# Kernel tuning notes

Hardware: AMD Instinct MI355X
Metric: run time of the kernel (lower is better)

Reference implementation:

```python
import jax, jax.numpy as jnp
import numpy as np

N = 8  # node_count, complete graph
# edge list exactly as in __init__: all (i, j) with i != j, row-major order
_edges = np.array([[i, j] for i in range(N) for j in range(N) if i != j], dtype=np.int32)
SRC = jnp.asarray(_edges[:, 0])  # edge_index[0]
DST = jnp.asarray(_edges[:, 1])  # edge_index[1]


def gcn_norm_adj(edge_w):
    """Dense normalized adjacency D^-1/2 (A + I) D^-1/2 with edge weights, as in PyG GCNConv."""
    A = jnp.zeros((N, N), edge_w.dtype).at[DST, SRC].set(edge_w) + jnp.eye(N, dtype=edge_w.dtype)
    deg = A.sum(axis=1)  # in-degree (weights into each target node, incl. self loop)
    dinv = jnp.where(deg > 0, deg ** -0.5, 0.0)
    return dinv[:, None] * A * dinv[None, :]


def setup_inputs() -> dict:
    key = jax.random.key(0)
    ks = jax.random.split(key, 4)
    B, F_, H, O = 8192, 512, 256, 128
    return {
        "latent_vec": jax.random.normal(ks[0], (B, F_), jnp.float32),
        "node_features": jax.random.normal(ks[1], (N, F_), jnp.float32) * 0.1,
        "edge_attr": jnp.ones((N * (N - 1), 1), jnp.float32),
        "W1": jax.random.normal(ks[2], (F_, H), jnp.float32) / np.sqrt(F_),
        "b1": jnp.zeros((H,), jnp.float32),
        "W2": jax.random.normal(ks[3], (H, O), jnp.float32) / np.sqrt(H),
        "b2": jnp.zeros((O,), jnp.float32),
    }


def reference(latent_vec, node_features, edge_attr, W1, b1, W2, b2):
    # update_graph_with_latent: per-sample softmax perturbation of shared node features
    w = jax.nn.softmax(latent_vec[:, :N], axis=1)[..., None]        # [B, N, 1]
    X = node_features[None, :, :] + 0.1 * w                          # [B, N, F]
    A_hat = gcn_norm_adj(edge_attr[:, 0])                            # [N, N], shared across batch
    # GCNConv1 + ReLU (dropout is identity in eval mode)
    h = jax.nn.relu(jnp.einsum('ij,bjh->bih', A_hat, X @ W1) + b1)   # [B, N, H]
    # GCNConv2
    o = jnp.einsum('ij,bjo->bio', A_hat, h @ W2) + b2                # [B, N, O]
    return o.mean(axis=1)                                            # [B, O]
```

## Files before the change

kernel.cpp:

```cpp
#include <hip/hip_runtime.h>

#define NNODE 8
#define FDIM 512
#define HDIM 256
#define ODIM 128
#define BATCH 8192
#define NEDGE (NNODE * (NNODE - 1))

#define FBLOCKS 8
#define FS (FDIM / FBLOCKS)
#define SPB 16


__global__ __launch_bounds__(256) void gnn_stage(const float* __restrict__ nf,
                                                 const float* __restrict__ W1,
                                                 float* __restrict__ ws) {
    const int k = blockIdx.x;
    const int t = threadIdx.x;
    __shared__ float nf_s[NNODE][FS];

    for (int idx = t; idx < NNODE * FS; idx += 256) {
        int n = idx / FS, f = idx % FS;
        nf_s[n][f] = nf[n * FDIM + k * FS + f];
    }
    __syncthreads();

    float s1 = 0.f;
    float y[NNODE];
#pragma unroll
    for (int n = 0; n < NNODE; n++) y[n] = 0.f;

    for (int ff = 0; ff < FS; ff++) {
        float wf = W1[(k * FS + ff) * HDIM + t];
        s1 += wf;
#pragma unroll
        for (int n = 0; n < NNODE; n++) y[n] = fmaf(nf_s[n][ff], wf, y[n]);
    }

    float* p = ws + (size_t)k * 9 * HDIM;
#pragma unroll
    for (int n = 0; n < NNODE; n++) p[n * HDIM + t] = y[n];
    p[8 * HDIM + t] = s1;
}

__global__ __launch_bounds__(256) void gnn_main(const float* __restrict__ latent,
                                                const float* __restrict__ edge_attr,
                                                const float* __restrict__ b1,
                                                const float* __restrict__ W2,
                                                const float* __restrict__ b2,
                                                const float* __restrict__ ws,
                                                float* __restrict__ out) {
    const int t = threadIdx.x;
    const int bs = blockIdx.x * SPB;

    __shared__ float Ahat_s[NNODE][NNODE];
    __shared__ float m_s[NNODE];
    __shared__ float w_s[SPB][NNODE];
    __shared__ float c_s[SPB][NNODE];
    __shared__ float g_s[SPB][HDIM];

    if (t == 0) {
        float A[NNODE][NNODE];
        for (int i = 0; i < NNODE; i++)
            for (int j = 0; j < NNODE; j++) A[i][j] = (i == j) ? 1.f : 0.f;
        for (int e = 0; e < NEDGE; e++) {
            int i = e / (NNODE - 1);
            int jj = e % (NNODE - 1);
            int j = jj + (jj >= i ? 1 : 0);
            A[j][i] += edge_attr[e];
        }
        float dinv[NNODE];
        for (int i = 0; i < NNODE; i++) {
            float d = 0.f;
            for (int j = 0; j < NNODE; j++) d += A[i][j];
            dinv[i] = d > 0.f ? 1.0f / sqrtf(d) : 0.f;
        }
        for (int i = 0; i < NNODE; i++)
            for (int j = 0; j < NNODE; j++) Ahat_s[i][j] = dinv[i] * A[i][j] * dinv[j];
        for (int j = 0; j < NNODE; j++) {
            float mm = 0.f;
            for (int i = 0; i < NNODE; i++) mm += Ahat_s[i][j];
            m_s[j] = mm * (1.0f / NNODE);
        }
    }

    if (t < SPB * NNODE) {
        int s = t >> 3, j = t & 7;
        w_s[s][j] = latent[(size_t)(bs + s) * FDIM + j];
    }
    __syncthreads();

    float wv = 0.f;
    if (t < SPB * NNODE) {
        int s = t >> 3, j = t & 7;
        float mx = -1e30f;
#pragma unroll
        for (int q = 0; q < NNODE; q++) mx = fmaxf(mx, w_s[s][q]);
        float sum = 0.f;
#pragma unroll
        for (int q = 0; q < NNODE; q++) sum += expf(w_s[s][q] - mx);
        wv = expf(w_s[s][j] - mx) / sum;
    }
    __syncthreads();
    if (t < SPB * NNODE) {
        int s = t >> 3, j = t & 7;
        w_s[s][j] = wv;
    }
    __syncthreads();

    if (t < SPB * NNODE) {
        int s = t >> 3, i = t & 7;
        float c = 0.f;
#pragma unroll
        for (int j = 0; j < NNODE; j++) c = fmaf(Ahat_s[i][j], w_s[s][j], c);
        c_s[s][i] = c;
    }
    __syncthreads();

    float Pj[NNODE];
    float s1t;
    {
        float y[NNODE];
        float s1 = 0.f;
#pragma unroll
        for (int n = 0; n < NNODE; n++) y[n] = 0.f;
        for (int k = 0; k < FBLOCKS; k++) {
            const float* p = ws + (size_t)k * 9 * HDIM;
#pragma unroll
            for (int n = 0; n < NNODE; n++) y[n] += p[n * HDIM + t];
            s1 += p[8 * HDIM + t];
        }
        s1t = s1;
        float bb = b1[t];
#pragma unroll
        for (int j = 0; j < NNODE; j++) {
            float acc = bb;
#pragma unroll
            for (int n = 0; n < NNODE; n++) acc = fmaf(Ahat_s[j][n], y[n], acc);
            Pj[j] = acc;
        }
    }

    {
        float s1t01 = 0.1f * s1t;
        float mreg[NNODE];
#pragma unroll
        for (int j = 0; j < NNODE; j++) mreg[j] = m_s[j];
        for (int s = 0; s < SPB; s++) {
            float g = 0.f;
#pragma unroll
            for (int j = 0; j < NNODE; j++) {
                float pre = fmaf(s1t01, c_s[s][j], Pj[j]);
                g = fmaf(mreg[j], fmaxf(pre, 0.f), g);
            }
            g_s[s][t] = g;
        }
    }
    __syncthreads();

    const int o = t & (ODIM - 1);
    const int grp = t >> 7;
    float acc[8];
#pragma unroll
    for (int k2 = 0; k2 < 8; k2++) acc[k2] = 0.f;

    for (int h = 0; h < HDIM; h += 4) {
        float w0 = W2[(h + 0) * ODIM + o];
        float w1 = W2[(h + 1) * ODIM + o];
        float w2v = W2[(h + 2) * ODIM + o];
        float w3 = W2[(h + 3) * ODIM + o];
#pragma unroll
        for (int k2 = 0; k2 < 8; k2++) {
            const float4 gv = *(const float4*)&g_s[grp * 8 + k2][h];
            acc[k2] = fmaf(gv.x, w0,
                      fmaf(gv.y, w1,
                      fmaf(gv.z, w2v,
                      fmaf(gv.w, w3, acc[k2]))));
        }
    }

    float bo = b2[o];
#pragma unroll
    for (int k2 = 0; k2 < 8; k2++) {
        out[(size_t)(bs + grp * 8 + k2) * ODIM + o] = acc[k2] + bo;
    }
}

extern "C" void kernel_launch(void* const* d_in, const int* in_sizes, int n_in,
                              void* d_out, int out_size, void* d_ws, size_t ws_size,
                              hipStream_t stream) {
    const float* latent = (const float*)d_in[0];
    const float* nf     = (const float*)d_in[1];
    const float* ea     = (const float*)d_in[2];
    const float* W1     = (const float*)d_in[3];
    const float* b1     = (const float*)d_in[4];
    const float* W2     = (const float*)d_in[5];
    const float* b2     = (const float*)d_in[6];
    float* out = (float*)d_out;
    float* ws  = (float*)d_ws;

    hipLaunchKernelGGL(gnn_stage, dim3(FBLOCKS), dim3(256), 0, stream, nf, W1, ws);
    hipLaunchKernelGGL(gnn_main, dim3(BATCH / SPB), dim3(256), 0, stream,
                       latent, ea, b1, W2, b2, ws, out);
}
```

Baseline: 29.05 us.

## Hoist batch-invariant GCN precompute into mid kernel and tile W2 GEMM in LDS

Adds a single-block kernel that computes the normalized adjacency, column means, the reduction of partial products and the bias-adjusted P terms once. Previously each of the 512 main blocks repeated this work, including a serial thread-0 adjacency build. The main kernel now loads these precomputed values, fuses softmax with the adjacency product, and runs the final GEMM with W2 tiles staged in shared memory. Each thread computes a 2-sample by 4-output tile with float4 loads and stores. The stage kernel is also split into more feature blocks. The cost is an extra launch and a serial single-block kernel, plus 32KB of LDS per main block, which may lower occupancy.

```diff
diff --git a/kernel.cpp b/kernel.cpp
--- a/kernel.cpp
+++ b/kernel.cpp
@@ -7,10 +7,15 @@
 #define BATCH 8192
 #define NEDGE (NNODE * (NNODE - 1))
 
-#define FBLOCKS 8
+#define FBLOCKS 16
 #define FS (FDIM / FBLOCKS)
 #define SPB 16
 
+#define WS2_OFF (FBLOCKS * 9 * HDIM)
+#define WS2_P 0
+#define WS2_S1 (8 * HDIM)
+#define WS2_A (WS2_S1 + HDIM)
+#define WS2_M (WS2_A + 64)
 
 __global__ __launch_bounds__(256) void gnn_stage(const float* __restrict__ nf,
                                                  const float* __restrict__ W1,
@@ -19,8 +24,8 @@
     const int t = threadIdx.x;
     __shared__ float nf_s[NNODE][FS];
 
-    for (int idx = t; idx < NNODE * FS; idx += 256) {
-        int n = idx / FS, f = idx % FS;
+    {
+        int n = t >> 5, f = t & 31;
         nf_s[n][f] = nf[n * FDIM + k * FS + f];
     }
     __syncthreads();
@@ -30,6 +35,7 @@
 #pragma unroll
     for (int n = 0; n < NNODE; n++) y[n] = 0.f;
 
+#pragma unroll
     for (int ff = 0; ff < FS; ff++) {
         float wf = W1[(k * FS + ff) * HDIM + t];
         s1 += wf;
@@ -43,22 +49,23 @@
     p[8 * HDIM + t] = s1;
 }
 
-__global__ __launch_bounds__(256) void gnn_main(const float* __restrict__ latent,
-                                                const float* __restrict__ edge_attr,
-                                                const float* __restrict__ b1,
-                                                const float* __restrict__ W2,
-                                                const float* __restrict__ b2,
-                                                const float* __restrict__ ws,
-                                                float* __restrict__ out) {
+__global__ __launch_bounds__(256) void gnn_mid(const float* __restrict__ edge_attr,
+                                               const float* __restrict__ b1,
+                                               float* __restrict__ ws) {
     const int t = threadIdx.x;
-    const int bs = blockIdx.x * SPB;
-
-    __shared__ float Ahat_s[NNODE][NNODE];
+    float y[NNODE];
+    float s1 = 0.f;
+#pragma unroll
+    for (int n = 0; n < NNODE; n++) y[n] = 0.f;
+    for (int k = 0; k < FBLOCKS; k++) {
+        const float* p = ws + (size_t)k * 9 * HDIM;
+#pragma unroll
+        for (int n = 0; n < NNODE; n++) y[n] += p[n * HDIM + t];
+        s1 += p[8 * HDIM + t];
+    }
+
+    __shared__ float A_s[NNODE * NNODE];
     __shared__ float m_s[NNODE];
-    __shared__ float w_s[SPB][NNODE];
-    __shared__ float c_s[SPB][NNODE];
-    __shared__ float g_s[SPB][HDIM];
-
     if (t == 0) {
         float A[NNODE][NNODE];
         for (int i = 0; i < NNODE; i++)
@@ -76,81 +83,85 @@
             dinv[i] = d > 0.f ? 1.0f / sqrtf(d) : 0.f;
         }
         for (int i = 0; i < NNODE; i++)
-            for (int j = 0; j < NNODE; j++) Ahat_s[i][j] = dinv[i] * A[i][j] * dinv[j];
+            for (int j = 0; j < NNODE; j++) A_s[i * NNODE + j] = dinv[i] * A[i][j] * dinv[j];
         for (int j = 0; j < NNODE; j++) {
             float mm = 0.f;
-            for (int i = 0; i < NNODE; i++) mm += Ahat_s[i][j];
+            for (int i = 0; i < NNODE; i++) mm += A_s[i * NNODE + j];
             m_s[j] = mm * (1.0f / NNODE);
         }
     }
-
-    if (t < SPB * NNODE) {
-        int s = t >> 3, j = t & 7;
-        w_s[s][j] = latent[(size_t)(bs + s) * FDIM + j];
-    }
-    __syncthreads();
-
-    float wv = 0.f;
-    if (t < SPB * NNODE) {
-        int s = t >> 3, j = t & 7;
-        float mx = -1e30f;
-#pragma unroll
-        for (int q = 0; q < NNODE; q++) mx = fmaxf(mx, w_s[s][q]);
-        float sum = 0.f;
-#pragma unroll
-        for (int q = 0; q < NNODE; q++) sum += expf(w_s[s][q] - mx);
-        wv = expf(w_s[s][j] - mx) / sum;
-    }
-    __syncthreads();
-    if (t < SPB * NNODE) {
-        int s = t >> 3, j = t & 7;
-        w_s[s][j] = wv;
-    }
+    __syncthreads();
+
+    float* w2 = ws + WS2_OFF;
+    float bb = b1[t];
+#pragma unroll
+    for (int j = 0; j < NNODE; j++) {
+        float acc = bb;
+#pragma unroll
+        for (int n = 0; n < NNODE; n++) acc = fmaf(A_s[j * NNODE + n], y[n], acc);
+        w2[WS2_P + j * HDIM + t] = acc;
+    }
+    w2[WS2_S1 + t] = s1;
+    if (t < NNODE * NNODE) w2[WS2_A + t] = A_s[t];
+    if (t < NNODE) w2[WS2_M + t] = m_s[t];
+}
+
+__global__ __launch_bounds__(256) void gnn_main(const float* __restrict__ latent,
+                                                const float* __restrict__ W2,
+                                                const float* __restrict__ b2,
+                                                const float* __restrict__ ws,
+                                                float* __restrict__ out) {
+    const int t = threadIdx.x;
+    const int bs = blockIdx.x * SPB;
+    const float* wsp = ws + WS2_OFF;
+
+    __shared__ float A_s[NNODE * NNODE];
+    __shared__ float m_s[NNODE];
+    __shared__ float lat_s[SPB][NNODE];
+    __shared__ float c_s[SPB][NNODE];
+    __shared__ float g_s[SPB][HDIM];
+    __shared__ float wt[64 * ODIM];
+
+    if (t < NNODE * NNODE) A_s[t] = wsp[WS2_A + t];
+    if (t >= 64 && t < 64 + NNODE) m_s[t - 64] = wsp[WS2_M + (t - 64)];
+    if (t >= 128 && t < 128 + SPB * NNODE) {
+        int u = t - 128;
+        int s = u >> 3, j = u & 7;
+        lat_s[s][j] = latent[(size_t)(bs + s) * FDIM + j];
+    }
+    float P[NNODE];
+#pragma unroll
+    for (int j = 0; j < NNODE; j++) P[j] = wsp[WS2_P + j * HDIM + t];
+    float s1t = wsp[WS2_S1 + t];
     __syncthreads();
 
     if (t < SPB * NNODE) {
         int s = t >> 3, i = t & 7;
-        float c = 0.f;
-#pragma unroll
-        for (int j = 0; j < NNODE; j++) c = fmaf(Ahat_s[i][j], w_s[s][j], c);
-        c_s[s][i] = c;
-    }
-    __syncthreads();
-
-    float Pj[NNODE];
-    float s1t;
+        float mx = -1e30f;
+#pragma unroll
+        for (int q = 0; q < NNODE; q++) mx = fmaxf(mx, lat_s[s][q]);
+        float sum = 0.f, acc = 0.f;
+#pragma unroll
+        for (int q = 0; q < NNODE; q++) {
+            float e = expf(lat_s[s][q] - mx);
+            sum += e;
+            acc = fmaf(A_s[i * NNODE + q], e, acc);
+        }
+        c_s[s][i] = acc / sum;
+    }
+    __syncthreads();
+
     {
-        float y[NNODE];
-        float s1 = 0.f;
-#pragma unroll
-        for (int n = 0; n < NNODE; n++) y[n] = 0.f;
-        for (int k = 0; k < FBLOCKS; k++) {
-            const float* p = ws + (size_t)k * 9 * HDIM;
-#pragma unroll
-            for (int n = 0; n < NNODE; n++) y[n] += p[n * HDIM + t];
-            s1 += p[8 * HDIM + t];
-        }
-        s1t = s1;
-        float bb = b1[t];
-#pragma unroll
-        for (int j = 0; j < NNODE; j++) {
-            float acc = bb;
-#pragma unroll
-            for (int n = 0; n < NNODE; n++) acc = fmaf(Ahat_s[j][n], y[n], acc);
-            Pj[j] = acc;
-        }
-    }
-
-    {
-        float s1t01 = 0.1f * s1t;
+        float s101 = 0.1f * s1t;
         float mreg[NNODE];
 #pragma unroll
         for (int j = 0; j < NNODE; j++) mreg[j] = m_s[j];
+#pragma unroll 4
         for (int s = 0; s < SPB; s++) {
             float g = 0.f;
 #pragma unroll
             for (int j = 0; j < NNODE; j++) {
-                float pre = fmaf(s1t01, c_s[s][j], Pj[j]);
+                float pre = fmaf(s101, c_s[s][j], P[j]);
                 g = fmaf(mreg[j], fmaxf(pre, 0.f), g);
             }
             g_s[s][t] = g;
@@ -158,32 +169,56 @@
     }
     __syncthreads();
 
-    const int o = t & (ODIM - 1);
-    const int grp = t >> 7;
-    float acc[8];
-#pragma unroll
-    for (int k2 = 0; k2 < 8; k2++) acc[k2] = 0.f;
-
-    for (int h = 0; h < HDIM; h += 4) {
-        float w0 = W2[(h + 0) * ODIM + o];
-        float w1 = W2[(h + 1) * ODIM + o];
-        float w2v = W2[(h + 2) * ODIM + o];
-        float w3 = W2[(h + 3) * ODIM + o];
-#pragma unroll
-        for (int k2 = 0; k2 < 8; k2++) {
-            const float4 gv = *(const float4*)&g_s[grp * 8 + k2][h];
-            acc[k2] = fmaf(gv.x, w0,
-                      fmaf(gv.y, w1,
-                      fmaf(gv.z, w2v,
-                      fmaf(gv.w, w3, acc[k2]))));
-        }
-    }
-
-    float bo = b2[o];
-#pragma unroll
-    for (int k2 = 0; k2 < 8; k2++) {
-        out[(size_t)(bs + grp * 8 + k2) * ODIM + o] = acc[k2] + bo;
-    }
+    const int oq = t & 31;
+    const int sg = t >> 5;
+    const int sa = sg * 2, sb = sg * 2 + 1;
+    float4 acc0 = {0.f, 0.f, 0.f, 0.f};
+    float4 acc1 = {0.f, 0.f, 0.f, 0.f};
+    const float4* W2v = (const float4*)W2;
+    float4* wtv = (float4*)wt;
+
+    for (int tile = 0; tile < HDIM / 64; ++tile) {
+#pragma unroll
+        for (int i = 0; i < 8; ++i)
+            wtv[t + 256 * i] = W2v[tile * 2048 + t + 256 * i];
+        __syncthreads();
+
+#pragma unroll
+        for (int hh = 0; hh < 64; hh += 4) {
+            const int hb = tile * 64 + hh;
+            float4 ga = *(const float4*)&g_s[sa][hb];
+            float4 gb = *(const float4*)&g_s[sb][hb];
+            float4 w0 = *(const float4*)&wt[(hh + 0) * ODIM + oq * 4];
+            float4 w1 = *(const float4*)&wt[(hh + 1) * ODIM + oq * 4];
+            float4 w2r = *(const float4*)&wt[(hh + 2) * ODIM + oq * 4];
+            float4 w3 = *(const float4*)&wt[(hh + 3) * ODIM + oq * 4];
+
+            acc0.x = fmaf(ga.x, w0.x, acc0.x); acc0.y = fmaf(ga.x, w0.y, acc0.y);
+            acc0.z = fmaf(ga.x, w0.z, acc0.z); acc0.w = fmaf(ga.x, w0.w, acc0.w);
+            acc0.x = fmaf(ga.y, w1.x, acc0.x); acc0.y = fmaf(ga.y, w1.y, acc0.y);
+            acc0.z = fmaf(ga.y, w1.z, acc0.z); acc0.w = fmaf(ga.y, w1.w, acc0.w);
+            acc0.x = fmaf(ga.z, w2r.x, acc0.x); acc0.y = fmaf(ga.z, w2r.y, acc0.y);
+            acc0.z = fmaf(ga.z, w2r.z, acc0.z); acc0.w = fmaf(ga.z, w2r.w, acc0.w);
+            acc0.x = fmaf(ga.w, w3.x, acc0.x); acc0.y = fmaf(ga.w, w3.y, acc0.y);
+            acc0.z = fmaf(ga.w, w3.z, acc0.z); acc0.w = fmaf(ga.w, w3.w, acc0.w);
+
+            acc1.x = fmaf(gb.x, w0.x, acc1.x); acc1.y = fmaf(gb.x, w0.y, acc1.y);
+            acc1.z = fmaf(gb.x, w0.z, acc1.z); acc1.w = fmaf(gb.x, w0.w, acc1.w);
+            acc1.x = fmaf(gb.y, w1.x, acc1.x); acc1.y = fmaf(gb.y, w1.y, acc1.y);
+            acc1.z = fmaf(gb.y, w1.z, acc1.z); acc1.w = fmaf(gb.y, w1.w, acc1.w);
+            acc1.x = fmaf(gb.z, w2r.x, acc1.x); acc1.y = fmaf(gb.z, w2r.y, acc1.y);
+            acc1.z = fmaf(gb.z, w2r.z, acc1.z); acc1.w = fmaf(gb.z, w2r.w, acc1.w);
+            acc1.x = fmaf(gb.w, w3.x, acc1.x); acc1.y = fmaf(gb.w, w3.y, acc1.y);
+            acc1.z = fmaf(gb.w, w3.z, acc1.z); acc1.w = fmaf(gb.w, w3.w, acc1.w);
+        }
+        __syncthreads();
+    }
+
+    float4 bo = *(const float4*)&b2[oq * 4];
+    acc0.x += bo.x; acc0.y += bo.y; acc0.z += bo.z; acc0.w += bo.w;
+    acc1.x += bo.x; acc1.y += bo.y; acc1.z += bo.z; acc1.w += bo.w;
+    *(float4*)&out[(size_t)(bs + sa) * ODIM + oq * 4] = acc0;
+    *(float4*)&out[(size_t)(bs + sb) * ODIM + oq * 4] = acc1;
 }
 
 extern "C" void kernel_launch(void* const* d_in, const int* in_sizes, int n_in,
@@ -200,6 +235,7 @@
     float* ws  = (float*)d_ws;
 
     hipLaunchKernelGGL(gnn_stage, dim3(FBLOCKS), dim3(256), 0, stream, nf, W1, ws);
+    hipLaunchKernelGGL(gnn_mid, dim3(1), dim3(256), 0, stream, ea, b1, ws);
     hipLaunchKernelGGL(gnn_main, dim3(BATCH / SPB), dim3(256), 0, stream,
-                       latent, ea, b1, W2, b2, ws, out);
-}
+                       latent, W2, b2, ws, out);
+}
```

Result: no change. 29.01 us (-0.1%).

## Precompute piecewise-linear ReLU breakpoint tables and replace per-sample GEMM with lookups

Applied to the files above, without the earlier changes.

Uses the fact that each hidden pre-activation is affine in a per-sample scalar c_j, so the ReLU pattern depends only on where c_j falls among 256 sorted breakpoints. A new build kernel sorts the breakpoints per node and precomputes prefix-sum tables of W2 contributions for every breakpoint interval. The main kernel then does a softmax, a binary search per node and eight table lookups per output instead of the 256x128 W2 matmul. This trades the main GEMM for a serial build kernel of only 8 blocks, a large workspace table and gather loads. The prefix accumulation over sorted breakpoints can also shift floating-point rounding.

```diff
diff --git a/kernel.cpp b/kernel.cpp
--- a/kernel.cpp
+++ b/kernel.cpp
@@ -5,12 +5,18 @@
 #define HDIM 256
 #define ODIM 128
 #define BATCH 8192
-#define NEDGE (NNODE * (NNODE - 1))
-
-#define FBLOCKS 8
+#define NEDGE 56
+#define FBLOCKS 16
 #define FS (FDIM / FBLOCKS)
 #define SPB 16
-
+#define NBLK (BATCH / SPB)
+
+#define OFF_PART 0
+#define OFF_TAU  (FBLOCKS * 9 * HDIM)
+#define OFF_AHAT (OFF_TAU + NNODE * HDIM)
+#define OFF_TABA (OFF_AHAT + 128)
+#define TABJ     (257 * ODIM)
+#define OFF_TABB (OFF_TABA + NNODE * TABJ)
 
 __global__ __launch_bounds__(256) void gnn_stage(const float* __restrict__ nf,
                                                  const float* __restrict__ W1,
@@ -19,8 +25,8 @@
     const int t = threadIdx.x;
     __shared__ float nf_s[NNODE][FS];
 
-    for (int idx = t; idx < NNODE * FS; idx += 256) {
-        int n = idx / FS, f = idx % FS;
+    {
+        int n = t >> 5, f = t & 31;
         nf_s[n][f] = nf[n * FDIM + k * FS + f];
     }
     __syncthreads();
@@ -30,6 +36,7 @@
 #pragma unroll
     for (int n = 0; n < NNODE; n++) y[n] = 0.f;
 
+#pragma unroll
     for (int ff = 0; ff < FS; ff++) {
         float wf = W1[(k * FS + ff) * HDIM + t];
         s1 += wf;
@@ -43,146 +50,179 @@
     p[8 * HDIM + t] = s1;
 }
 
+__global__ __launch_bounds__(256) void gnn_build(const float* __restrict__ ea,
+                                                 const float* __restrict__ b1,
+                                                 const float* __restrict__ W2,
+                                                 float* __restrict__ ws) {
+    const int j = blockIdx.x;
+    const int t = threadIdx.x;
+    __shared__ float ea_s[NEDGE];
+    __shared__ float A_s[64];
+    __shared__ float P_s[HDIM];
+    __shared__ float k_s[HDIM];
+    __shared__ float tau_s[HDIM];
+    __shared__ int   hs[HDIM];
+    __shared__ float mj_sh;
+
+    if (t < NEDGE) ea_s[t] = ea[t];
+
+    float y[NNODE];
+    float s1 = 0.f;
+#pragma unroll
+    for (int n = 0; n < NNODE; n++) y[n] = 0.f;
+#pragma unroll 4
+    for (int k = 0; k < FBLOCKS; k++) {
+        const float* p = ws + (size_t)k * 9 * HDIM;
+#pragma unroll
+        for (int n = 0; n < NNODE; n++) y[n] += p[n * HDIM + t];
+        s1 += p[8 * HDIM + t];
+    }
+    __syncthreads();
+
+    if (t == 0) {
+        float A[NNODE][NNODE];
+        for (int i = 0; i < NNODE; i++)
+            for (int q = 0; q < NNODE; q++) A[i][q] = (i == q) ? 1.f : 0.f;
+        for (int e = 0; e < NEDGE; e++) {
+            int i = e / (NNODE - 1);
+            int qq = e % (NNODE - 1);
+            int q = qq + (qq >= i ? 1 : 0);
+            A[q][i] += ea_s[e];
+        }
+        float dinv[NNODE];
+        for (int i = 0; i < NNODE; i++) {
+            float d = 0.f;
+            for (int q = 0; q < NNODE; q++) d += A[i][q];
+            dinv[i] = d > 0.f ? 1.0f / sqrtf(d) : 0.f;
+        }
+        for (int i = 0; i < NNODE; i++)
+            for (int q = 0; q < NNODE; q++) A_s[i * NNODE + q] = dinv[i] * A[i][q] * dinv[q];
+        float mm = 0.f;
+        for (int r = 0; r < NNODE; r++) mm += A_s[r * NNODE + j];
+        mj_sh = mm * (1.0f / NNODE);
+    }
+    __syncthreads();
+
+    float P = b1[t];
+#pragma unroll
+    for (int n = 0; n < NNODE; n++) P = fmaf(A_s[j * NNODE + n], y[n], P);
+    float kap = 0.1f * s1;
+    float tau = (kap != 0.f) ? (-P / kap) : __builtin_inff();
+    P_s[t] = P;
+    k_s[t] = kap;
+    tau_s[t] = tau;
+    __syncthreads();
+
+    {
+        int r = 0;
+        for (int k = 0; k < HDIM; k++) {
+            float tk = tau_s[k];
+            r += (tk < tau) || (tk == tau && k < t);
+        }
+        hs[r] = t;
+        ws[OFF_TAU + j * HDIM + r] = tau;
+    }
+    if (j == 0 && t < 64) ws[OFF_AHAT + t] = A_s[t];
+    __syncthreads();
+
+    if (t < ODIM) {
+        const int o = t;
+        const float mj = mj_sh;
+        float a0 = 0.f, b0 = 0.f;
+#pragma unroll 4
+        for (int h = 0; h < HDIM; h++) {
+            float w2v = W2[h * ODIM + o];
+            float kk = k_s[h], pp = P_s[h];
+            if (kk < 0.f) {
+                a0 = fmaf(pp, w2v, a0);
+                b0 = fmaf(kk, w2v, b0);
+            } else if (kk == 0.f && pp > 0.f) {
+                a0 = fmaf(pp, w2v, a0);
+            }
+        }
+        float* TA = ws + OFF_TABA + (size_t)j * TABJ;
+        float* TB = ws + OFF_TABB + (size_t)j * TABJ;
+        TA[o] = mj * a0;
+        TB[o] = mj * b0;
+#pragma unroll 2
+        for (int r = 0; r < HDIM; r++) {
+            int e = hs[r];
+            float kk = k_s[e], pp = P_s[e];
+            float sgn = (kk > 0.f) ? 1.f : ((kk < 0.f) ? -1.f : 0.f);
+            float w2v = W2[e * ODIM + o];
+            a0 = fmaf(sgn * pp, w2v, a0);
+            b0 = fmaf(sgn * kk, w2v, b0);
+            TA[(size_t)(r + 1) * ODIM + o] = mj * a0;
+            TB[(size_t)(r + 1) * ODIM + o] = mj * b0;
+        }
+    }
+}
+
 __global__ __launch_bounds__(256) void gnn_main(const float* __restrict__ latent,
-                                                const float* __restrict__ edge_attr,
-                                                const float* __restrict__ b1,
-                                                const float* __restrict__ W2,
                                                 const float* __restrict__ b2,
                                                 const float* __restrict__ ws,
                                                 float* __restrict__ out) {
     const int t = threadIdx.x;
     const int bs = blockIdx.x * SPB;
 
-    __shared__ float Ahat_s[NNODE][NNODE];
-    __shared__ float m_s[NNODE];
-    __shared__ float w_s[SPB][NNODE];
-    __shared__ float c_s[SPB][NNODE];
-    __shared__ float g_s[SPB][HDIM];
-
-    if (t == 0) {
-        float A[NNODE][NNODE];
-        for (int i = 0; i < NNODE; i++)
-            for (int j = 0; j < NNODE; j++) A[i][j] = (i == j) ? 1.f : 0.f;
-        for (int e = 0; e < NEDGE; e++) {
-            int i = e / (NNODE - 1);
-            int jj = e % (NNODE - 1);
-            int j = jj + (jj >= i ? 1 : 0);
-            A[j][i] += edge_attr[e];
-        }
-        float dinv[NNODE];
-        for (int i = 0; i < NNODE; i++) {
-            float d = 0.f;
-            for (int j = 0; j < NNODE; j++) d += A[i][j];
-            dinv[i] = d > 0.f ? 1.0f / sqrtf(d) : 0.f;
-        }
-        for (int i = 0; i < NNODE; i++)
-            for (int j = 0; j < NNODE; j++) Ahat_s[i][j] = dinv[i] * A[i][j] * dinv[j];
-        for (int j = 0; j < NNODE; j++) {
-            float mm = 0.f;
-            for (int i = 0; i < NNODE; i++) mm += Ahat_s[i][j];
-            m_s[j] = mm * (1.0f / NNODE);
-        }
-    }
-
-    if (t < SPB * NNODE) {
-        int s = t >> 3, j = t & 7;
-        w_s[s][j] = latent[(size_t)(bs + s) * FDIM + j];
-    }
-    __syncthreads();
-
-    float wv = 0.f;
-    if (t < SPB * NNODE) {
-        int s = t >> 3, j = t & 7;
-        float mx = -1e30f;
-#pragma unroll
-        for (int q = 0; q < NNODE; q++) mx = fmaxf(mx, w_s[s][q]);
-        float sum = 0.f;
-#pragma unroll
-        for (int q = 0; q < NNODE; q++) sum += expf(w_s[s][q] - mx);
-        wv = expf(w_s[s][j] - mx) / sum;
-    }
-    __syncthreads();
-    if (t < SPB * NNODE) {
-        int s = t >> 3, j = t & 7;
-        w_s[s][j] = wv;
+    __shared__ float tau_s[NNODE][HDIM];
+    __shared__ float A_s[64];
+    __shared__ float lat_s[SPB][NNODE];
+    __shared__ float cc_s[SPB][NNODE];
+    __shared__ int   rr_s[SPB][NNODE];
+
+    for (int k = t; k < NNODE * HDIM; k += 256)
+        ((float*)tau_s)[k] = ws[OFF_TAU + k];
+    if (t < 64) A_s[t] = ws[OFF_AHAT + t];
+    if (t >= 128) {
+        int u = t - 128;
+        int s = u >> 3, q = u & 7;
+        lat_s[s][q] = latent[(size_t)(bs + s) * FDIM + q];
     }
     __syncthreads();
 
     if (t < SPB * NNODE) {
         int s = t >> 3, i = t & 7;
-        float c = 0.f;
-#pragma unroll
-        for (int j = 0; j < NNODE; j++) c = fmaf(Ahat_s[i][j], w_s[s][j], c);
-        c_s[s][i] = c;
-    }
-    __syncthreads();
-
-    float Pj[NNODE];
-    float s1t;
-    {
-        float y[NNODE];
-        float s1 = 0.f;
-#pragma unroll
-        for (int n = 0; n < NNODE; n++) y[n] = 0.f;
-        for (int k = 0; k < FBLOCKS; k++) {
-            const float* p = ws + (size_t)k * 9 * HDIM;
-#pragma unroll
-            for (int n = 0; n < NNODE; n++) y[n] += p[n * HDIM + t];
-            s1 += p[8 * HDIM + t];
-        }
-        s1t = s1;
-        float bb = b1[t];
+        float mx = -1e30f;
+#pragma unroll
+        for (int q = 0; q < NNODE; q++) mx = fmaxf(mx, lat_s[s][q]);
+        float sum = 0.f, acc = 0.f;
+#pragma unroll
+        for (int q = 0; q < NNODE; q++) {
+            float e = expf(lat_s[s][q] - mx);
+            sum += e;
+            acc = fmaf(A_s[i * NNODE + q], e, acc);
+        }
+        float c = acc / sum;
+        cc_s[s][i] = c;
+        int lo = 0, hi = HDIM;
+        while (lo < hi) {
+            int mid = (lo + hi) >> 1;
+            if (tau_s[i][mid] < c) lo = mid + 1; else hi = mid;
+        }
+        rr_s[s][i] = lo;
+    }
+    __syncthreads();
+
+    const int o = t & (ODIM - 1);
+    const int sh = t >> 7;
+    const float* TA = ws + OFF_TABA;
+    const float* TB = ws + OFF_TABB;
+    const float bo = b2[o];
+
+#pragma unroll 2
+    for (int s = sh; s < SPB; s += 2) {
+        float acc = bo;
 #pragma unroll
         for (int j = 0; j < NNODE; j++) {
-            float acc = bb;
-#pragma unroll
-            for (int n = 0; n < NNODE; n++) acc = fmaf(Ahat_s[j][n], y[n], acc);
-            Pj[j] = acc;
-        }
-    }
-
-    {
-        float s1t01 = 0.1f * s1t;
-        float mreg[NNODE];
-#pragma unroll
-        for (int j = 0; j < NNODE; j++) mreg[j] = m_s[j];
-        for (int s = 0; s < SPB; s++) {
-            float g = 0.f;
-#pragma unroll
-            for (int j = 0; j < NNODE; j++) {
-                float pre = fmaf(s1t01, c_s[s][j], Pj[j]);
-                g = fmaf(mreg[j], fmaxf(pre, 0.f), g);
-            }
-            g_s[s][t] = g;
-        }
-    }
-    __syncthreads();
-
-    const int o = t & (ODIM - 1);
-    const int grp = t >> 7;
-    float acc[8];
-#pragma unroll
-    for (int k2 = 0; k2 < 8; k2++) acc[k2] = 0.f;
-
-    for (int h = 0; h < HDIM; h += 4) {
-        float w0 = W2[(h + 0) * ODIM + o];
-        float w1 = W2[(h + 1) * ODIM + o];
-        float w2v = W2[(h + 2) * ODIM + o];
-        float w3 = W2[(h + 3) * ODIM + o];
-#pragma unroll
-        for (int k2 = 0; k2 < 8; k2++) {
-            const float4 gv = *(const float4*)&g_s[grp * 8 + k2][h];
-            acc[k2] = fmaf(gv.x, w0,
-                      fmaf(gv.y, w1,
-                      fmaf(gv.z, w2v,
-                      fmaf(gv.w, w3, acc[k2]))));
-        }
-    }
-
-    float bo = b2[o];
-#pragma unroll
-    for (int k2 = 0; k2 < 8; k2++) {
-        out[(size_t)(bs + grp * 8 + k2) * ODIM + o] = acc[k2] + bo;
+            int r = rr_s[s][j];
+            float c = cc_s[s][j];
+            size_t base = (size_t)j * TABJ + (size_t)r * ODIM + o;
+            float av = TA[base];
+            float bv = TB[base];
+            acc += fmaf(c, bv, av);
+        }
+        out[(size_t)(bs + s) * ODIM + o] = acc;
     }
 }
 
@@ -200,6 +240,6 @@
     float* ws  = (float*)d_ws;
 
     hipLaunchKernelGGL(gnn_stage, dim3(FBLOCKS), dim3(256), 0, stream, nf, W1, ws);
-    hipLaunchKernelGGL(gnn_main, dim3(BATCH / SPB), dim3(256), 0, stream,
-                       latent, ea, b1, W2, b2, ws, out);
-}
+    hipLaunchKernelGGL(gnn_build, dim3(NNODE), dim3(256), 0, stream, ea, b1, W2, ws);
+    hipLaunchKernelGGL(gnn_main, dim3(NBLK), dim3(256), 0, stream, latent, b2, ws, out);
+}
```

Result: slower. 75.88 us (+161.2%).
